# Kernel tuning notes

Measured on AMD Instinct MI355X. Metric: run time of the kernel, lower is better.

Reference implementation:

```python
import jax, jax.numpy as jnp
import numpy as np

N_QUERY, N_BACKGND, DIM = 2048, 8192, 32


def setup_inputs() -> dict:
    key = jax.random.key(0)
    k0, k1, k2, k3 = jax.random.split(key, 4)
    x_backgnd = jax.random.normal(k0, (N_BACKGND, DIM), dtype=jnp.float32)
    y_backgnd = jax.random.normal(k1, (N_BACKGND,), dtype=jnp.float32)
    x_query = jax.random.normal(k2, (N_QUERY, DIM), dtype=jnp.float32)
    r = jax.random.uniform(k3, (N_QUERY, N_BACKGND), dtype=jnp.float32)
    sigma = jnp.array([0.1], dtype=jnp.float32)      # nn.Parameter init_sigma
    r_scale = jnp.array([3.0], dtype=jnp.float32)    # nn.Parameter init_r_scale
    w = jnp.ones((DIM,), dtype=jnp.float32)          # trainable weights matrix
    return {"x_backgnd": x_backgnd, "y_backgnd": y_backgnd, "x_query": x_query,
            "r": r, "sigma": sigma, "r_scale": r_scale, "w": w}


def reference(x_backgnd, y_backgnd, x_query, r, sigma, r_scale, w):
    # weighted Euclidean distance: ||(xq - xb) * w|| via the expansion trick,
    # avoiding the (n_query, n_backgnd, dim) difference tensor.
    xq = x_query * w           # (nq, d)
    xb = x_backgnd * w         # (nb, d)
    q2 = jnp.sum(xq * xq, axis=1, keepdims=True)        # (nq, 1)
    b2 = jnp.sum(xb * xb, axis=1)                        # (nb,)
    d2 = q2 + b2[None, :] - 2.0 * (xq @ xb.T)            # (nq, nb)
    dists = jnp.sqrt(jnp.maximum(d2, 0.0))
    # exp kernel with relationship bias, normalize, weighted sum
    k_vals = jnp.exp(-dists / sigma + r_scale * r)       # sigma, r_scale broadcast (1,)
    k_sum = jnp.sum(k_vals, axis=1, keepdims=True) + 1e-8
    weights = k_vals / k_sum
    y_pred = weights @ y_backgnd                          # (nq,)
    return y_pred
```

## Files before the change

kernel.cpp:

```cpp
#include <hip/hip_runtime.h>
#include <math.h>

#define NQ 2048
#define NB 8192
#define DIM 32

#define LOG2E 1.44269504088896340736f

typedef _Float16 half8 __attribute__((ext_vector_type(8)));
typedef float    f32x4 __attribute__((ext_vector_type(4)));

#define NCHUNK 64
#define WS_PSK  0
#define WS_PSKY (NCHUNK * NQ * 4)
#define WS_Q2   (2 * NCHUNK * NQ * 4)
#define WS_B2   (WS_Q2 + NQ * 4)
#define WS_XQH  (WS_B2 + NB * 4)
#define WS_XBH  (WS_XQH + NQ * DIM * 2)

__global__ __launch_bounds__(256) void relnw_pre(
    const float* __restrict__ xq, const float* __restrict__ xb,
    const float* __restrict__ w,
    _Float16* __restrict__ XQh, _Float16* __restrict__ XBh,
    float* __restrict__ q2, float* __restrict__ b2)
{
    const int tid = threadIdx.x;
    const int row = blockIdx.x * 64 + (tid >> 2);
    const int p   = tid & 3;
    if (row >= NQ + NB) return;

    const float* src; _Float16* dst; float* s2; float scale;
    if (row < NQ) { src = xq + (size_t)row * DIM;
                    dst = XQh + (size_t)row * DIM; s2 = q2 + row; scale = 1.f; }
    else          { int j = row - NQ;
                    src = xb + (size_t)j * DIM;
                    dst = XBh + (size_t)j * DIM;   s2 = b2 + j;   scale = -2.f; }

    const float4 xa  = ((const float4*)src)[p * 2];
    const float4 xbv = ((const float4*)src)[p * 2 + 1];
    const float4 wa  = ((const float4*)w)[p * 2];
    const float4 wb  = ((const float4*)w)[p * 2 + 1];
    const float xs[8]  = {xa.x, xa.y, xa.z, xa.w, xbv.x, xbv.y, xbv.z, xbv.w};
    const float ws_[8] = {wa.x, wa.y, wa.z, wa.w, wb.x, wb.y, wb.z, wb.w};

    half8 h;
    float s = 0.f;
#pragma unroll
    for (int c = 0; c < 8; ++c) {
        float t = xs[c] * ws_[c];
        _Float16 hh = (_Float16)t;
        float th = (float)hh;
        s = fmaf(th, th, s);
        h[c] = (_Float16)(th * scale);
    }
    *(half8*)(dst + p * 8) = h;

    s += __shfl_xor(s, 1, 64);
    s += __shfl_xor(s, 2, 64);
    if (p == 0) *s2 = s;
}

#define BT_PER_WAVE 8
#define BG_PER_WAVE (BT_PER_WAVE * 16)

__global__ __launch_bounds__(256) void relnw_main(
    const _Float16* __restrict__ XQh,
    const _Float16* __restrict__ XBh,
    const float* __restrict__ q2,
    const float* __restrict__ b2,
    const float* __restrict__ yb,
    const float* __restrict__ r,
    const float* __restrict__ sigma,
    const float* __restrict__ rscale,
    float* __restrict__ psk,
    float* __restrict__ psky)
{
    const int tid  = threadIdx.x;
    const int lane = tid & 63;
    const int wid  = tid >> 6;
    const int m    = lane & 15;
    const int quad = lane >> 4;

    const int q0     = blockIdx.y * 16;
    const int chunk  = blockIdx.x * 4 + wid;
    const int bstart = chunk * BG_PER_WAVE;

    const float c1 = -LOG2E / sigma[0];
    const float c2 =  LOG2E * rscale[0];

    const half8 afrag = *(const half8*)(XQh + (size_t)(q0 + m) * DIM + quad * 8);

    float q2r[4];
#pragma unroll
    for (int g = 0; g < 4; ++g) q2r[g] = q2[q0 + quad * 4 + g];

    const _Float16* xbp = XBh + (size_t)(bstart + m) * DIM + quad * 8;

    const float* rbase[4];
#pragma unroll
    for (int g = 0; g < 4; ++g)
        rbase[g] = r + (size_t)(q0 + quad * 4 + g) * NB + bstart + m;

    float sk[4]  = {0.f, 0.f, 0.f, 0.f};
    float sky[4] = {0.f, 0.f, 0.f, 0.f};

#pragma unroll
    for (int it = 0; it < BT_PER_WAVE; ++it) {
        const int bc = bstart + it * 16 + m;
        const half8 bfrag = *(const half8*)(xbp + (size_t)it * 16 * DIM);
        const float yv  = yb[bc];
        const float b2v = b2[bc];
        float rr[4];
#pragma unroll
        for (int g = 0; g < 4; ++g) rr[g] = rbase[g][it * 16];

        f32x4 cin;
#pragma unroll
        for (int g = 0; g < 4; ++g) cin[g] = q2r[g] + b2v;

        f32x4 d2v = __builtin_amdgcn_mfma_f32_16x16x32_f16(
            afrag, bfrag, cin, 0, 0, 0);

#pragma unroll
        for (int g = 0; g < 4; ++g) {
            float d2 = fmaxf(d2v[g], 0.f);
            float dist = __builtin_amdgcn_sqrtf(d2);
            float e = fmaf(dist, c1, rr[g] * c2);
            float k = __builtin_amdgcn_exp2f(e);
            sk[g] += k;
            sky[g] = fmaf(k, yv, sky[g]);
        }
    }

#pragma unroll
    for (int off = 1; off <= 8; off <<= 1) {
#pragma unroll
        for (int g = 0; g < 4; ++g) {
            sk[g]  += __shfl_xor(sk[g],  off, 64);
            sky[g] += __shfl_xor(sky[g], off, 64);
        }
    }
    if (m == 0) {
        f32x4 vk  = {sk[0],  sk[1],  sk[2],  sk[3]};
        f32x4 vky = {sky[0], sky[1], sky[2], sky[3]};
        *(f32x4*)(psk  + (size_t)chunk * NQ + q0 + quad * 4) = vk;
        *(f32x4*)(psky + (size_t)chunk * NQ + q0 + quad * 4) = vky;
    }
}

__global__ __launch_bounds__(256) void relnw_finalize(
    const float* __restrict__ psk, const float* __restrict__ psky,
    float* __restrict__ out)
{
    int q = blockIdx.x * 256 + threadIdx.x;
    float sk = 0.f, sky = 0.f;
#pragma unroll 8
    for (int c = 0; c < NCHUNK; ++c) {
        sk  += psk[(size_t)c * NQ + q];
        sky += psky[(size_t)c * NQ + q];
    }
    out[q] = sky / (sk + 1e-8f);
}

extern "C" void kernel_launch(void* const* d_in, const int* in_sizes, int n_in,
                              void* d_out, int out_size, void* d_ws, size_t ws_size,
                              hipStream_t stream) {
    const float* xb     = (const float*)d_in[0];
    const float* yb     = (const float*)d_in[1];
    const float* xq     = (const float*)d_in[2];
    const float* r      = (const float*)d_in[3];
    const float* sigma  = (const float*)d_in[4];
    const float* rscale = (const float*)d_in[5];
    const float* w      = (const float*)d_in[6];
    float* out = (float*)d_out;

    char* ws = (char*)d_ws;
    float*    psk  = (float*)(ws + WS_PSK);
    float*    psky = (float*)(ws + WS_PSKY);
    float*    q2   = (float*)(ws + WS_Q2);
    float*    b2   = (float*)(ws + WS_B2);
    _Float16* XQh  = (_Float16*)(ws + WS_XQH);
    _Float16* XBh  = (_Float16*)(ws + WS_XBH);

    relnw_pre<<<(NQ + NB) / 64, 256, 0, stream>>>(xq, xb, w, XQh, XBh, q2, b2);

    dim3 grid(NB / (4 * BG_PER_WAVE), NQ / 16);
    relnw_main<<<grid, 256, 0, stream>>>(XQh, XBh, q2, b2, yb, r, sigma, rscale,
                                         psk, psky);

    relnw_finalize<<<NQ / 256, 256, 0, stream>>>(psk, psky, out);
}
```

Baseline: 116.4 us.

## Transpose MFMA operands so each lane owns a query row with vectorized r loads

Swaps the MFMA operand roles so the background tile is the A operand and the query tile is B. Each lane then accumulates a single query's partial sums, and r, b2 and y are read as contiguous float4 vectors instead of strided scalar loads. The cross-lane reduction shrinks from four butterfly rounds over eight values to two rounds over two values. Each wave also covers twice as many background tiles, which halves the chunk count and the finalize work but leaves fewer waves in the main grid.

```diff
diff --git a/kernel.cpp b/kernel.cpp
--- a/kernel.cpp
+++ b/kernel.cpp
@@ -10,7 +10,7 @@
 typedef _Float16 half8 __attribute__((ext_vector_type(8)));
 typedef float    f32x4 __attribute__((ext_vector_type(4)));
 
-#define NCHUNK 64
+#define NCHUNK 32
 #define WS_PSK  0
 #define WS_PSKY (NCHUNK * NQ * 4)
 #define WS_Q2   (2 * NCHUNK * NQ * 4)
@@ -60,7 +60,7 @@
     if (p == 0) *s2 = s;
 }
 
-#define BT_PER_WAVE 8
+#define BT_PER_WAVE 16
 #define BG_PER_WAVE (BT_PER_WAVE * 16)
 
 __global__ __launch_bounds__(256) void relnw_main(
@@ -88,63 +88,49 @@
     const float c1 = -LOG2E / sigma[0];
     const float c2 =  LOG2E * rscale[0];
 
-    const half8 afrag = *(const half8*)(XQh + (size_t)(q0 + m) * DIM + quad * 8);
-
-    float q2r[4];
-#pragma unroll
-    for (int g = 0; g < 4; ++g) q2r[g] = q2[q0 + quad * 4 + g];
+    const half8 qfrag = *(const half8*)(XQh + (size_t)(q0 + m) * DIM + quad * 8);
+    const float q2m   = q2[q0 + m];
 
     const _Float16* xbp = XBh + (size_t)(bstart + m) * DIM + quad * 8;
 
-    const float* rbase[4];
-#pragma unroll
-    for (int g = 0; g < 4; ++g)
-        rbase[g] = r + (size_t)(q0 + quad * 4 + g) * NB + bstart + m;
+    const float* rrow = r + (size_t)(q0 + m) * NB + bstart + quad * 4;
 
-    float sk[4]  = {0.f, 0.f, 0.f, 0.f};
-    float sky[4] = {0.f, 0.f, 0.f, 0.f};
+    float sk = 0.f, sky = 0.f;
 
 #pragma unroll
     for (int it = 0; it < BT_PER_WAVE; ++it) {
-        const int bc = bstart + it * 16 + m;
-        const half8 bfrag = *(const half8*)(xbp + (size_t)it * 16 * DIM);
-        const float yv  = yb[bc];
-        const float b2v = b2[bc];
-        float rr[4];
-#pragma unroll
-        for (int g = 0; g < 4; ++g) rr[g] = rbase[g][it * 16];
+        const half8 afrag = *(const half8*)(xbp + (size_t)it * 16 * DIM);
+        const int   bq    = bstart + it * 16 + quad * 4;
+        const f32x4 rr4   = *(const f32x4*)(rrow + it * 16);
+        const f32x4 b2v4  = *(const f32x4*)(b2 + bq);
+        const f32x4 yv4   = *(const f32x4*)(yb + bq);
 
         f32x4 cin;
 #pragma unroll
-        for (int g = 0; g < 4; ++g) cin[g] = q2r[g] + b2v;
+        for (int g = 0; g < 4; ++g) cin[g] = q2m + b2v4[g];
 
         f32x4 d2v = __builtin_amdgcn_mfma_f32_16x16x32_f16(
-            afrag, bfrag, cin, 0, 0, 0);
+            afrag, qfrag, cin, 0, 0, 0);
 
 #pragma unroll
         for (int g = 0; g < 4; ++g) {
             float d2 = fmaxf(d2v[g], 0.f);
             float dist = __builtin_amdgcn_sqrtf(d2);
-            float e = fmaf(dist, c1, rr[g] * c2);
+            float e = fmaf(dist, c1, rr4[g] * c2);
             float k = __builtin_amdgcn_exp2f(e);
-            sk[g] += k;
-            sky[g] = fmaf(k, yv, sky[g]);
+            sk += k;
+            sky = fmaf(k, yv4[g], sky);
         }
     }
 
-#pragma unroll
-    for (int off = 1; off <= 8; off <<= 1) {
-#pragma unroll
-        for (int g = 0; g < 4; ++g) {
-            sk[g]  += __shfl_xor(sk[g],  off, 64);
-            sky[g] += __shfl_xor(sky[g], off, 64);
-        }
-    }
-    if (m == 0) {
-        f32x4 vk  = {sk[0],  sk[1],  sk[2],  sk[3]};
-        f32x4 vky = {sky[0], sky[1], sky[2], sky[3]};
-        *(f32x4*)(psk  + (size_t)chunk * NQ + q0 + quad * 4) = vk;
-        *(f32x4*)(psky + (size_t)chunk * NQ + q0 + quad * 4) = vky;
+    sk  += __shfl_xor(sk,  16, 64);
+    sky += __shfl_xor(sky, 16, 64);
+    sk  += __shfl_xor(sk,  32, 64);
+    sky += __shfl_xor(sky, 32, 64);
+
+    if (quad == 0) {
+        psk [(size_t)chunk * NQ + q0 + m] = sk;
+        psky[(size_t)chunk * NQ + q0 + m] = sky;
     }
 }
 
```

Result: slower. 120.4 us (+3.4%).
